# Kernel optimization log

Hardware: AMD Instinct MI355X
Metric: run time of the kernel (lower is better)

Reference implementation:

```python
import jax, jax.numpy as jnp
import numpy as np

N, C, G, M, E = 100000, 8, 8, 32, 1600000
EPS = 1e-8


def setup_inputs() -> dict:
    key = jax.random.key(0)
    k1, k2, k3, k4, k5 = jax.random.split(key, 5)
    x = jax.random.randint(k1, (N,), 0, M)
    prev_h = jax.random.uniform(k2, (N, C, G), dtype=jnp.float32)
    edge_index = jax.random.randint(k3, (2, E), 0, N)
    Q_neigh = jax.random.normal(k4, (C, C, G), dtype=jnp.float32) * 1.25
    B = jax.random.normal(k5, (C, M, G), dtype=jnp.float32) * 1.25
    return {"x": x, "prev_h": prev_h, "edge_index": edge_index,
            "Q_neigh": Q_neigh, "B": B}


def reference(x, prev_h, edge_index, Q_neigh, B):
    n = prev_h.shape[0]
    # softmax reparameterization (vectorized over n_gen)
    Qs = jax.nn.softmax(Q_neigh, axis=0)          # [C, C, G], columns sum to 1 over dim 0
    Bs = jax.nn.softmax(B, axis=1)                # [C, M, G], rows sum to 1 over M

    dst, src = edge_index[0], edge_index[1]
    neigh = prev_h[src]                            # [E, C, G] gather
    summed = jax.ops.segment_sum(neigh, dst, num_segments=n)            # [N, C, G]
    counts = jax.ops.segment_sum(jnp.ones((src.shape[0],), prev_h.dtype), dst,
                                 num_segments=n)                        # [N]
    aggr = summed / jnp.maximum(counts, 1.0)[:, None, None]             # scatter-mean, 0 for isolated nodes

    B_nodes = jnp.transpose(Bs[:, x], (1, 0, 2))[:, :, None, :]         # [N, C, 1, G]
    unnorm = B_nodes * (Qs[None, :, :, :] * aggr[:, None, :, :]) + EPS  # [N, C, C, G]

    denom = unnorm.sum(axis=(1, 2), keepdims=True)                      # [N, 1, 1, G]
    posterior_il = unnorm / denom
    posterior_i = posterior_il.sum(axis=2)                              # [N, C, G]
    likelihood = jnp.log(jnp.squeeze(denom, (1, 2)))                    # [N, G]
    return likelihood, posterior_i
```

## Files before the change

kernel.cpp:

```cpp
#include <hip/hip_runtime.h>

#define C_    8
#define G_    8
#define CG    64
#define CAP   48
#define CELL  56
#define BSPAN 256
#define SBLK  256
#define CVT   160
#define Z1    488
#define Z2    480
#define ZTOT  4096
#define EPSF  1e-8f

__device__ __forceinline__ unsigned short bf16rne(float v) {
    unsigned u = __float_as_uint(v);
    return (unsigned short)((u + 0x7FFFu + ((u >> 16) & 1u)) >> 16);
}
__device__ __forceinline__ float bf16tof(unsigned short h) {
    return __uint_as_float((unsigned)h << 16);
}

__device__ __forceinline__ void zsum_block(int zgid, const float* __restrict__ Bmat,
                                           float* __restrict__ Z, int M) {
    if (zgid >= ZTOT) return;
    __shared__ float zpart[4][8];
    int c = zgid & 7, bx = zgid >> 3;
    const float4* B4 = (const float4*)(Bmat + (size_t)c * M * G_);
    const int total4 = M * 2;
    int tid = bx * 256 + threadIdx.x;
    const int zstride = (ZTOT / 8) * 256;
    float a0 = 0.f, a1 = 0.f, a2 = 0.f, a3 = 0.f;
    for (int f = tid; f < total4; f += zstride) {
        float4 v = B4[f];
        a0 += __expf(v.x); a1 += __expf(v.y); a2 += __expf(v.z); a3 += __expf(v.w);
    }
    #pragma unroll
    for (int m = 2; m <= 32; m <<= 1) {
        a0 += __shfl_xor(a0, m, 64);
        a1 += __shfl_xor(a1, m, 64);
        a2 += __shfl_xor(a2, m, 64);
        a3 += __shfl_xor(a3, m, 64);
    }
    int lane = threadIdx.x & 63, w = threadIdx.x >> 6;
    if (lane < 2) {
        int g0 = lane * 4;
        zpart[w][g0 + 0] = a0; zpart[w][g0 + 1] = a1;
        zpart[w][g0 + 2] = a2; zpart[w][g0 + 3] = a3;
    }
    __syncthreads();
    if (threadIdx.x < 8) {
        float s = zpart[0][threadIdx.x] + zpart[1][threadIdx.x]
                + zpart[2][threadIdx.x] + zpart[3][threadIdx.x];
        atomicAdd(&Z[c * G_ + threadIdx.x], s);
    }
}

__global__ void k_d1(const int* __restrict__ ei, int E, int npart,
                     int* __restrict__ counts, int* __restrict__ staging,
                     const float* __restrict__ prev_h, unsigned short* __restrict__ ph16,
                     int N, const float* __restrict__ Qn, float* __restrict__ Qs,
                     const float* __restrict__ Bmat, float* __restrict__ Z, int M) {
    int b = blockIdx.x;
    if (b < SBLK) {
        __shared__ int cur[512];
        for (int p = threadIdx.x; p < npart; p += 256) cur[p] = 0;
        __syncthreads();
        int chunk = (E + SBLK - 1) / SBLK;
        int lo = b * chunk, hi = min(E, lo + chunk);
        for (int e = lo + threadIdx.x; e < hi; e += 256) {
            int dst = ei[e], src = ei[E + e];
            int p = dst >> 8;
            int c = atomicAdd(&cur[p], 1);
            if (c < CELL) staging[(p * SBLK + b) * CELL + c] = ((dst & 255) << 23) | src;
        }
        __syncthreads();
        for (int p = threadIdx.x; p < npart; p += 256)
            counts[p * SBLK + b] = cur[p];
    } else if (b < SBLK + CVT) {
        int gid = (b - SBLK) * 256 + threadIdx.x;
        int total8 = N * 8;
        const int cstride = CVT * 256;
        for (int f = gid; f < total8; f += cstride) {
            const float4* s = (const float4*)(prev_h + (size_t)f * 8);
            float4 v0 = s[0], v1 = s[1];
            float vv[8] = {v0.x, v0.y, v0.z, v0.w, v1.x, v1.y, v1.z, v1.w};
            unsigned r[4];
            #pragma unroll
            for (int k = 0; k < 4; ++k)
                r[k] = (unsigned)bf16rne(vv[2 * k]) | ((unsigned)bf16rne(vv[2 * k + 1]) << 16);
            *(uint4*)(ph16 + (size_t)f * 8) = make_uint4(r[0], r[1], r[2], r[3]);
        }
    } else if (b == SBLK + CVT) {
        __shared__ float e[512];
        __shared__ float cs[64];
        int t = threadIdx.x;
        e[t] = __expf(Qn[t]); e[t + 256] = __expf(Qn[t + 256]);
        __syncthreads();
        if (t < 64) {
            float s = 0.f;
            #pragma unroll
            for (int i2 = 0; i2 < 8; ++i2) s += e[i2 * 64 + t];
            cs[t] = s;
        }
        __syncthreads();
        Qs[t] = e[t] / cs[t & 63];
        Qs[t + 256] = e[t + 256] / cs[t & 63];
    } else {
        zsum_block(b - (SBLK + CVT + 1), Bmat, Z, M);
    }
}

__global__ void k_d2(const int* __restrict__ counts, const int* __restrict__ staging,
                     int* __restrict__ cnt, int* __restrict__ csr, int N, int npart,
                     const float* __restrict__ Bmat, float* __restrict__ Z, int M) {
    int b = blockIdx.x;
    if (b >= npart) { zsum_block(Z1 + (b - npart), Bmat, Z, M); return; }
    __shared__ int cl[BSPAN];
    __shared__ int csl[BSPAN * CAP];
    int t = threadIdx.x;
    cl[t] = 0;
    __syncthreads();
    int cnum = min(counts[b * SBLK + t], CELL);
    int cbase = (b * SBLK + t) * CELL;
    for (int j = 0; j < cnum; ++j) {
        int v = staging[cbase + j];
        int local = (unsigned)v >> 23;
        int src = v & 0x7FFFFF;
        int pos = atomicAdd(&cl[local], 1);
        if (pos < CAP) csl[local * CAP + pos] = src;
    }
    __syncthreads();
    int n = b * BSPAN + t;
    if (n < N) cnt[n] = cl[t];
    for (int idx = t; idx < BSPAN * CAP; idx += 256)
        csr[(size_t)b * (BSPAN * CAP) + idx] = csl[idx];
}

__global__ void k_ti(const unsigned short* __restrict__ ph16, const int* __restrict__ cnt,
                     const int* __restrict__ csr, const float* __restrict__ Qs,
                     unsigned short* __restrict__ ti16, const int* __restrict__ x,
                     const float* __restrict__ Bmat, unsigned short* __restrict__ blog16,
                     float* __restrict__ Z, int M, int N, int ngroups) {
    int grp = blockIdx.x / 13, r = blockIdx.x % 13;
    int lane = threadIdx.x & 63, w = threadIdx.x >> 6;
    int i = lane >> 3, g = lane & 7;
    if (r < 8) {
        int a = grp * 8 + r;
        int base = a * 16 + w * 4;
        if (base >= N) return;
        int nk[4]; bool valid[4]; int deg[4], dl[4], nb[4];
        #pragma unroll
        for (int k = 0; k < 4; ++k) {
            int n = base + k;
            valid[k] = (n < N);
            nk[k] = valid[k] ? n : (N - 1);
        }
        #pragma unroll
        for (int k = 0; k < 4; ++k) {
            deg[k] = valid[k] ? cnt[nk[k]] : 0;
            dl[k]  = min(deg[k], CAP);
            nb[k]  = dl[k] >> 2;
        }
        float q[8];
        #pragma unroll
        for (int l = 0; l < 8; ++l) q[l] = Qs[i * 64 + l * 8 + g];
        float acc[4] = {0.f, 0.f, 0.f, 0.f};
        int nbmax = max(max(nb[0], nb[1]), max(nb[2], nb[3]));
        for (int q2 = 0; q2 < nbmax; ++q2) {
            #pragma unroll
            for (int k = 0; k < 4; ++k) {
                if (q2 < nb[k]) {
                    int4 s4 = ((const int4*)(csr + (size_t)nk[k] * CAP))[q2];
                    acc[k] += bf16tof(ph16[(s4.x << 6) | lane]);
                    acc[k] += bf16tof(ph16[(s4.y << 6) | lane]);
                    acc[k] += bf16tof(ph16[(s4.z << 6) | lane]);
                    acc[k] += bf16tof(ph16[(s4.w << 6) | lane]);
                }
            }
        }
        #pragma unroll
        for (int k = 0; k < 4; ++k) {
            const int* crow = csr + (size_t)nk[k] * CAP;
            for (int e2 = nb[k] * 4; e2 < dl[k]; ++e2)
                acc[k] += bf16tof(ph16[(crow[e2] << 6) | lane]);
        }
        #pragma unroll
        for (int k = 0; k < 4; ++k) {
            float aggr = (deg[k] > 0) ? acc[k] / (float)deg[k] : 0.f;
            float ti = 0.f;
            #pragma unroll
            for (int l = 0; l < 8; ++l) ti += q[l] * __shfl(aggr, l * 8 + g, 64);
            if (valid[k]) ti16[(size_t)nk[k] * CG + lane] = bf16rne(ti);
        }
    } else if (r == 8) {
        const int step = ngroups * 16;
        for (int n0 = (grp * 4 + w) * 4; n0 < N; n0 += step) {
            int xs[4];
            #pragma unroll
            for (int k = 0; k < 4; ++k) xs[k] = (n0 + k < N) ? x[n0 + k] : 0;
            #pragma unroll
            for (int k = 0; k < 4; ++k)
                if (n0 + k < N)
                    blog16[(size_t)(n0 + k) * CG + lane] =
                        bf16rne(Bmat[((size_t)i * M + xs[k]) * G_ + g]);
        }
    } else {
        zsum_block(Z1 + Z2 + grp * 4 + (r - 9), Bmat, Z, M);
    }
}

__global__ void k_epi(const unsigned short* __restrict__ ti16,
                      const unsigned short* __restrict__ blog16,
                      const float* __restrict__ Z, float* __restrict__ out, int N) {
    int w = threadIdx.x >> 6, lane = threadIdx.x & 63;
    int i = lane >> 3, g = lane & 7;
    int base = (blockIdx.x * 4 + w) * 4;
    if (base >= N) return;
    float invZ = 1.f / Z[lane];
    #pragma unroll
    for (int k = 0; k < 4; ++k) {
        int n = base + k;
        if (n >= N) break;
        float ti = bf16tof(ti16[(size_t)n * CG + lane]);
        float bl = bf16tof(blog16[(size_t)n * CG + lane]);
        float u = __expf(bl) * invZ * ti;
        float s = u;
        #pragma unroll
        for (int m = 8; m <= 32; m <<= 1) s += __shfl_xor(s, m, 64);
        float denom = s + 64.f * EPSF;
        if (i == 0) out[n * G_ + g] = logf(denom);
        out[(size_t)N * G_ + (size_t)n * CG + lane] = (u + 8.f * EPSF) / denom;
    }
}

extern "C" void kernel_launch(void* const* d_in, const int* in_sizes, int n_in,
                              void* d_out, int out_size, void* d_ws, size_t ws_size,
                              hipStream_t stream) {
    const int*   x      = (const int*)d_in[0];
    const float* prev_h = (const float*)d_in[1];
    const int*   ei     = (const int*)d_in[2];
    const float* Qn     = (const float*)d_in[3];
    const float* Bm     = (const float*)d_in[4];
    float* out = (float*)d_out;

    int N = in_sizes[0];
    int E = in_sizes[2] / 2;
    int M = in_sizes[4] / CG;
    int npart = (N + BSPAN - 1) / BSPAN;

    int nblk16  = (N + 15) / 16;
    int ngroups = (nblk16 + 7) / 8;
    int zg      = (ZTOT - Z1 - Z2 + 3) / 4;
    if (ngroups < zg) ngroups = zg;

    float* Z      = (float*)d_ws;
    float* Qs     = Z + 64;
    int*   counts = (int*)d_ws + 576;
    int*   cnt    = counts + npart * SBLK;
    int*   stag   = cnt + N;
    int*   csr    = stag + (size_t)npart * SBLK * CELL;
    unsigned short* ph16   = (unsigned short*)(csr + (size_t)npart * BSPAN * CAP);
    unsigned short* blog16 = ph16 + (size_t)N * CG;
    unsigned short* ti16   = blog16 + (size_t)N * CG;

    hipMemsetAsync(d_ws, 0, 64 * sizeof(float), stream);

    k_d1<<<SBLK + CVT + 1 + Z1, 256, 0, stream>>>(ei, E, npart, counts, stag,
                                                  prev_h, ph16, N, Qn, Qs, Bm, Z, M);
    k_d2<<<npart + Z2, 256, 0, stream>>>(counts, stag, cnt, csr, N, npart, Bm, Z, M);
    k_ti<<<ngroups * 13, 256, 0, stream>>>(ph16, cnt, csr, Qs, ti16, x, Bm, blog16,
                                           Z, M, N, ngroups);
    k_epi<<<(N + 15) / 16, 256, 0, stream>>>(ti16, blog16, Z, out, N);
}
```

Measured before the change: 137.6 us.

## Transpose bf16 prev_h layout and gather neighbor rows with 16-byte loads

The bf16 copy of prev_h is now stored transposed per node, and a zero sentinel row is appended. CSR rows are padded with the sentinel index so no tail loop is needed. In the aggregation kernel, each lane group of 8 handles one neighbor and loads a full 16-byte chunk per lane instead of one 2-byte element per lane. Partial sums are then reduced across the 8 edge slots with xor-shuffles and a select tree. This cuts the number of gather instructions and removes per-element scattered loads, at the cost of extra shuffles, padded work on short rows, and a less coalesced conversion write.

```diff
diff --git a/kernel.cpp b/kernel.cpp
--- a/kernel.cpp
+++ b/kernel.cpp
@@ -20,6 +20,8 @@
 __device__ __forceinline__ float bf16tof(unsigned short h) {
     return __uint_as_float((unsigned)h << 16);
 }
+__device__ __forceinline__ float bflo(unsigned u) { return __uint_as_float(u << 16); }
+__device__ __forceinline__ float bfhi(unsigned u) { return __uint_as_float(u & 0xFFFF0000u); }
 
 __device__ __forceinline__ void zsum_block(int zgid, const float* __restrict__ Bmat,
                                            float* __restrict__ Z, int M) {
@@ -78,19 +80,14 @@
         for (int p = threadIdx.x; p < npart; p += 256)
             counts[p * SBLK + b] = cur[p];
     } else if (b < SBLK + CVT) {
-        int gid = (b - SBLK) * 256 + threadIdx.x;
-        int total8 = N * 8;
-        const int cstride = CVT * 256;
-        for (int f = gid; f < total8; f += cstride) {
-            const float4* s = (const float4*)(prev_h + (size_t)f * 8);
-            float4 v0 = s[0], v1 = s[1];
-            float vv[8] = {v0.x, v0.y, v0.z, v0.w, v1.x, v1.y, v1.z, v1.w};
-            unsigned r[4];
-            #pragma unroll
-            for (int k = 0; k < 4; ++k)
-                r[k] = (unsigned)bf16rne(vv[2 * k]) | ((unsigned)bf16rne(vv[2 * k + 1]) << 16);
-            *(uint4*)(ph16 + (size_t)f * 8) = make_uint4(r[0], r[1], r[2], r[3]);
-        }
+        int lane = threadIdx.x & 63, w = threadIdx.x >> 6;
+        int f = (lane & 7) * 8 + (lane >> 3);
+        int wid = (b - SBLK) * 4 + w;
+        const int wstep = CVT * 4;
+        for (int n = wid; n < N; n += wstep)
+            ph16[(size_t)n * CG + lane] = bf16rne(prev_h[(size_t)n * CG + f]);
+        if (b == SBLK && threadIdx.x < 64)
+            ph16[(size_t)N * CG + threadIdx.x] = 0;
     } else if (b == SBLK + CVT) {
         __shared__ float e[512];
         __shared__ float cs[64];
@@ -133,8 +130,11 @@
     __syncthreads();
     int n = b * BSPAN + t;
     if (n < N) cnt[n] = cl[t];
-    for (int idx = t; idx < BSPAN * CAP; idx += 256)
-        csr[(size_t)b * (BSPAN * CAP) + idx] = csl[idx];
+    for (int idx = t; idx < BSPAN * CAP; idx += 256) {
+        int local = idx / CAP, pos = idx - local * CAP;
+        csr[(size_t)b * (BSPAN * CAP) + idx] =
+            (pos < min(cl[local], CAP)) ? csl[idx] : N;
+    }
 }
 
 __global__ void k_ti(const unsigned short* __restrict__ ph16, const int* __restrict__ cnt,
@@ -149,7 +149,9 @@
         int a = grp * 8 + r;
         int base = a * 16 + w * 4;
         if (base >= N) return;
-        int nk[4]; bool valid[4]; int deg[4], dl[4], nb[4];
+        int es = lane >> 3;
+        int ch = lane & 7;
+        int nk[4]; bool valid[4]; int deg[4], ng[4];
         #pragma unroll
         for (int k = 0; k < 4; ++k) {
             int n = base + k;
@@ -159,35 +161,48 @@
         #pragma unroll
         for (int k = 0; k < 4; ++k) {
             deg[k] = valid[k] ? cnt[nk[k]] : 0;
-            dl[k]  = min(deg[k], CAP);
-            nb[k]  = dl[k] >> 2;
-        }
-        float q[8];
-        #pragma unroll
-        for (int l = 0; l < 8; ++l) q[l] = Qs[i * 64 + l * 8 + g];
-        float acc[4] = {0.f, 0.f, 0.f, 0.f};
-        int nbmax = max(max(nb[0], nb[1]), max(nb[2], nb[3]));
-        for (int q2 = 0; q2 < nbmax; ++q2) {
+            ng[k]  = (min(deg[k], CAP) + 7) >> 3;
+        }
+        float acc[4][8];
+        #pragma unroll
+        for (int k = 0; k < 4; ++k)
+            #pragma unroll
+            for (int j = 0; j < 8; ++j) acc[k][j] = 0.f;
+        int ngmax = max(max(ng[0], ng[1]), max(ng[2], ng[3]));
+        for (int t2 = 0; t2 < ngmax; ++t2) {
             #pragma unroll
             for (int k = 0; k < 4; ++k) {
-                if (q2 < nb[k]) {
-                    int4 s4 = ((const int4*)(csr + (size_t)nk[k] * CAP))[q2];
-                    acc[k] += bf16tof(ph16[(s4.x << 6) | lane]);
-                    acc[k] += bf16tof(ph16[(s4.y << 6) | lane]);
-                    acc[k] += bf16tof(ph16[(s4.z << 6) | lane]);
-                    acc[k] += bf16tof(ph16[(s4.w << 6) | lane]);
+                if (t2 < ng[k]) {
+                    int src = csr[(size_t)nk[k] * CAP + t2 * 8 + es];
+                    const uint4* p = (const uint4*)(ph16 + ((size_t)src << 6) + (ch << 3));
+                    uint4 v = *p;
+                    acc[k][0] += bflo(v.x); acc[k][1] += bfhi(v.x);
+                    acc[k][2] += bflo(v.y); acc[k][3] += bfhi(v.y);
+                    acc[k][4] += bflo(v.z); acc[k][5] += bfhi(v.z);
+                    acc[k][6] += bflo(v.w); acc[k][7] += bfhi(v.w);
                 }
             }
         }
+        float q[8];
+        #pragma unroll
+        for (int l = 0; l < 8; ++l) q[l] = Qs[i * 64 + l * 8 + g];
         #pragma unroll
         for (int k = 0; k < 4; ++k) {
-            const int* crow = csr + (size_t)nk[k] * CAP;
-            for (int e2 = nb[k] * 4; e2 < dl[k]; ++e2)
-                acc[k] += bf16tof(ph16[(crow[e2] << 6) | lane]);
-        }
-        #pragma unroll
-        for (int k = 0; k < 4; ++k) {
-            float aggr = (deg[k] > 0) ? acc[k] / (float)deg[k] : 0.f;
+            #pragma unroll
+            for (int j = 0; j < 8; ++j) {
+                acc[k][j] += __shfl_xor(acc[k][j], 8, 64);
+                acc[k][j] += __shfl_xor(acc[k][j], 16, 64);
+                acc[k][j] += __shfl_xor(acc[k][j], 32, 64);
+            }
+            int b3 = lane >> 3;
+            float s01 = (b3 & 1) ? acc[k][1] : acc[k][0];
+            float s23 = (b3 & 1) ? acc[k][3] : acc[k][2];
+            float s45 = (b3 & 1) ? acc[k][5] : acc[k][4];
+            float s67 = (b3 & 1) ? acc[k][7] : acc[k][6];
+            float s03 = (b3 & 2) ? s23 : s01;
+            float s47 = (b3 & 2) ? s67 : s45;
+            float asum = (b3 & 4) ? s47 : s03;
+            float aggr = (deg[k] > 0) ? asum / (float)deg[k] : 0.f;
             float ti = 0.f;
             #pragma unroll
             for (int l = 0; l < 8; ++l) ti += q[l] * __shfl(aggr, l * 8 + g, 64);
@@ -254,15 +269,19 @@
     int zg      = (ZTOT - Z1 - Z2 + 3) / 4;
     if (ngroups < zg) ngroups = zg;
 
+    auto align32 = [](size_t v) { return (v + 31) & ~(size_t)31; };
     float* Z      = (float*)d_ws;
     float* Qs     = Z + 64;
-    int*   counts = (int*)d_ws + 576;
-    int*   cnt    = counts + npart * SBLK;
-    int*   stag   = cnt + N;
-    int*   csr    = stag + (size_t)npart * SBLK * CELL;
-    unsigned short* ph16   = (unsigned short*)(csr + (size_t)npart * BSPAN * CAP);
-    unsigned short* blog16 = ph16 + (size_t)N * CG;
-    unsigned short* ti16   = blog16 + (size_t)N * CG;
+    size_t off    = align32(64 + 512);
+    int*   counts = (int*)d_ws + off;              off = align32(off + (size_t)npart * SBLK);
+    int*   cnt    = (int*)d_ws + off;              off = align32(off + (size_t)N);
+    int*   stag   = (int*)d_ws + off;              off = align32(off + (size_t)npart * SBLK * CELL);
+    int*   csr    = (int*)d_ws + off;              off = align32(off + (size_t)npart * BSPAN * CAP);
+    unsigned short* ph16   = (unsigned short*)((int*)d_ws + off);
+    off = align32(off + ((size_t)(N + 1) * CG + 1) / 2);
+    unsigned short* blog16 = (unsigned short*)((int*)d_ws + off);
+    off = align32(off + ((size_t)N * CG + 1) / 2);
+    unsigned short* ti16   = (unsigned short*)((int*)d_ws + off);
 
     hipMemsetAsync(d_ws, 0, 64 * sizeof(float), stream);
 
```

After: 206.3 us. +49.9%, slower.
